# Kernel tuning notes

Measured on AMD Instinct MI355X. Metric: run time of the kernel, lower is better.

## Reference

```python
import jax, jax.numpy as jnp
import numpy as np

STD = 0.5
B = 1048576
DIM = 8  # arch == 2
_LOG_STD = -0.6931471805599453       # log(0.5)
_HALF_LOG_2PI = 0.9189385332046727   # 0.5*log(2*pi)


def _mlp(x, w1, b1, w2, b2):
    # Sequential(Linear, ReLU, Linear)
    return jnp.maximum(x @ w1 + b1, 0.0) @ w2 + b2


def _bce_sum(logits, targets):
    # BCEWithLogitsLoss(reduction='sum'), numerically stable
    return jnp.sum(jnp.maximum(logits, 0.0) - logits * targets
                   + jnp.log1p(jnp.exp(-jnp.abs(logits))))


def _normal_logprob_sum(mu, y):
    # D.Normal(mu, STD).log_prob(y).sum()
    return jnp.sum(-0.5 * ((y - mu) / STD) ** 2 - _LOG_STD - _HALF_LOG_2PI)


def setup_inputs() -> dict:
    key = jax.random.key(0)
    keys = iter(jax.random.split(key, 64))

    def nrm(shape, s=1.0):
        return s * jax.random.normal(next(keys), shape, dtype=jnp.float32)

    inp = {
        'y1': nrm((B, 1)),
        'y2': nrm((B, 1)),
        'n1': jax.random.uniform(next(keys), (B, 2), dtype=jnp.float32),
        'n2': jax.random.uniform(next(keys), (B, 2), dtype=jnp.float32),
        'n3': jax.random.uniform(next(keys), (B, 2), dtype=jnp.float32),
        'n4': jax.random.uniform(next(keys), (B, 2), dtype=jnp.float32),
    }
    # (name, d_in, d_out) for every 2-layer MLP in infnet/gennet
    mlp_specs = [('inf0', 2, 2), ('inf1', 3, 2), ('inf2', 1, 2), ('inf3', 2, 2),
                 ('g1', 2, 2), ('g2', 2, 1), ('g3', 1, 2), ('g4', 2, 2), ('g5', 2, 1)]
    for name, din, dout in mlp_specs:
        inp[name + '_w1'] = nrm((din, DIM), 0.5)
        inp[name + '_b1'] = nrm((DIM,), 0.1)
        inp[name + '_w2'] = nrm((DIM, dout), 0.5)
        inp[name + '_b2'] = nrm((dout,), 0.1)
    inp['g0_w'] = nrm((1, 2), 0.5)  # gennet[0]: Linear(1, z, bias=False)
    return inp


def reference(y1, y2, n1, n2, n3, n4,
              inf0_w1, inf0_b1, inf0_w2, inf0_b2,
              inf1_w1, inf1_b1, inf1_w2, inf1_b2,
              inf2_w1, inf2_b1, inf2_w2, inf2_b2,
              inf3_w1, inf3_b1, inf3_w2, inf3_b2,
              g1_w1, g1_b1, g1_w2, g1_b2,
              g2_w1, g2_b1, g2_w2, g2_b2,
              g3_w1, g3_b1, g3_w2, g3_b2,
              g4_w1, g4_b1, g4_w2, g4_b2,
              g5_w1, g5_b1, g5_w2, g5_b2,
              g0_w):
    b = y1.shape[0]
    # ---- infer(): recognition pass with hard Bernoulli samples ----
    pz1 = jax.nn.sigmoid(_mlp(jnp.concatenate([y1, y2], axis=1),
                              inf0_w1, inf0_b1, inf0_w2, inf0_b2))
    z1 = (pz1 > n1).astype(jnp.float32)
    pz2 = jax.nn.sigmoid(_mlp(jnp.concatenate([y2, z1], axis=1),
                              inf1_w1, inf1_b1, inf1_w2, inf1_b2))
    z2 = (pz2 > n2).astype(jnp.float32)
    pz3 = jax.nn.sigmoid(_mlp(y2, inf2_w1, inf2_b1, inf2_w2, inf2_b2))
    z3 = (pz3 > n3).astype(jnp.float32)
    pz4 = jax.nn.sigmoid(_mlp(z3, inf3_w1, inf3_b1, inf3_w2, inf3_b2))
    z4 = (pz4 > n4).astype(jnp.float32)
    # ---- generate_wake(): generative logits conditioned on inferred latents ----
    l4 = jnp.ones((b, 1), jnp.float32) @ g0_w          # [B, 2]
    l3 = _mlp(z4, g1_w1, g1_b1, g1_w2, g1_b2)          # [B, 2]
    muy2 = _mlp(z3, g2_w1, g2_b1, g2_w2, g2_b2)        # [B, 1]
    l2 = _mlp(y2, g3_w1, g3_b1, g3_w2, g3_b2)          # [B, 2]
    l1 = _mlp(z2, g4_w1, g4_b1, g4_w2, g4_b2)          # [B, 2]
    muy1 = _mlp(z1, g5_w1, g5_b1, g5_w2, g5_b2)        # [B, 1]
    # ---- wake losses ----
    bf = jnp.float32(b)
    loss_z = (_bce_sum(l1, z1) + _bce_sum(l2, z2)
              + _bce_sum(l3, z3) + _bce_sum(l4, z4)) / bf
    loss_y = (-_normal_logprob_sum(muy1, y1)
              - _normal_logprob_sum(muy2, y2)) / bf
    return (loss_z + loss_y, loss_z, loss_y)
```

## Files before the change

kernel.cpp:

```cpp
#include <hip/hip_runtime.h>

#define NB 1024
#define NT 256

__device__ __forceinline__ float bce_f(float l, float t) {
    float e = __expf(-fabsf(l));
    return fmaxf(l, 0.0f) - l * t + __logf(1.0f + e);
}

__device__ __forceinline__ float z_from(float s, float n) {
    float e = __expf(-s);
    return (1.0f - n > n * e) ? 1.0f : 0.0f;
}

__global__ __launch_bounds__(NT) void wake_main(
    const float* __restrict__ y1, const float* __restrict__ y2,
    const float* __restrict__ n1, const float* __restrict__ n2,
    const float* __restrict__ n3, const float* __restrict__ n4,
    const float* __restrict__ i0w1, const float* __restrict__ i0b1,
    const float* __restrict__ i0w2, const float* __restrict__ i0b2,
    const float* __restrict__ i1w1, const float* __restrict__ i1b1,
    const float* __restrict__ i1w2, const float* __restrict__ i1b2,
    const float* __restrict__ i2w1, const float* __restrict__ i2b1,
    const float* __restrict__ i2w2, const float* __restrict__ i2b2,
    const float* __restrict__ i3w1, const float* __restrict__ i3b1,
    const float* __restrict__ i3w2, const float* __restrict__ i3b2,
    const float* __restrict__ g1w1, const float* __restrict__ g1b1,
    const float* __restrict__ g1w2, const float* __restrict__ g1b2,
    const float* __restrict__ g2w1, const float* __restrict__ g2b1,
    const float* __restrict__ g2w2, const float* __restrict__ g2b2,
    const float* __restrict__ g3w1, const float* __restrict__ g3b1,
    const float* __restrict__ g3w2, const float* __restrict__ g3b2,
    const float* __restrict__ g4w1, const float* __restrict__ g4b1,
    const float* __restrict__ g4w2, const float* __restrict__ g4b2,
    const float* __restrict__ g5w1, const float* __restrict__ g5b1,
    const float* __restrict__ g5w2, const float* __restrict__ g5b2,
    const float* __restrict__ g0w,
    float2* __restrict__ partials)
{
    __shared__ float lds_eval[5][4][2];
    __shared__ float lds_coef[40];

    const int tid = threadIdx.x;
    const int g = blockIdx.x * NT + tid;

    const float4 vy1  = reinterpret_cast<const float4*>(y1)[g];
    const float4 vy2  = reinterpret_cast<const float4*>(y2)[g];
    const float4 n1lo = reinterpret_cast<const float4*>(n1)[2*g];
    const float4 n1hi = reinterpret_cast<const float4*>(n1)[2*g+1];
    const float4 n2lo = reinterpret_cast<const float4*>(n2)[2*g];
    const float4 n2hi = reinterpret_cast<const float4*>(n2)[2*g+1];
    const float4 n3lo = reinterpret_cast<const float4*>(n3)[2*g];
    const float4 n3hi = reinterpret_cast<const float4*>(n3)[2*g+1];
    const float4 n4lo = reinterpret_cast<const float4*>(n4)[2*g];
    const float4 n4hi = reinterpret_cast<const float4*>(n4)[2*g+1];

    if (tid < 20) {
        const int m = tid >> 2, c = tid & 3;
        const float z0 = (float)(c & 1), z1f = (float)(c >> 1);
        const float *w1, *bb1, *w2, *bb2; int dout;
        switch (m) {
            case 0:  w1 = i3w1; bb1 = i3b1; w2 = i3w2; bb2 = i3b2; dout = 2; break;
            case 1:  w1 = g1w1; bb1 = g1b1; w2 = g1w2; bb2 = g1b2; dout = 2; break;
            case 2:  w1 = g2w1; bb1 = g2b1; w2 = g2w2; bb2 = g2b2; dout = 1; break;
            case 3:  w1 = g4w1; bb1 = g4b1; w2 = g4w2; bb2 = g4b2; dout = 2; break;
            default: w1 = g5w1; bb1 = g5b1; w2 = g5w2; bb2 = g5b2; dout = 1; break;
        }
        float o0 = bb2[0];
        float o1 = (dout == 2) ? bb2[1] : 0.0f;
        #pragma unroll
        for (int j = 0; j < 8; ++j) {
            float h = fmaxf(bb1[j] + z0 * w1[j] + z1f * w1[8 + j], 0.0f);
            o0 += h * w2[j * dout];
            if (dout == 2) o1 += h * w2[j * 2 + 1];
        }
        lds_eval[m][c][0] = o0;
        lds_eval[m][c][1] = o1;
    }
    __syncthreads();
    if (tid < 10) {
        const int m = tid >> 1, k = tid & 1;
        const float f00 = lds_eval[m][0][k], f10 = lds_eval[m][1][k];
        const float f01 = lds_eval[m][2][k], f11 = lds_eval[m][3][k];
        lds_coef[tid * 4 + 0] = f00;
        lds_coef[tid * 4 + 1] = f10 - f00;
        lds_coef[tid * 4 + 2] = f01 - f00;
        lds_coef[tid * 4 + 3] = f11 - f10 - f01 + f00;
    }
    __syncthreads();

    const float l40 = g0w[0], l41 = g0w[1];

    const float Y1a[4] = {vy1.x, vy1.y, vy1.z, vy1.w};
    const float Y2a[4] = {vy2.x, vy2.y, vy2.z, vy2.w};
    const float N1a[8] = {n1lo.x, n1lo.y, n1lo.z, n1lo.w, n1hi.x, n1hi.y, n1hi.z, n1hi.w};
    const float N2a[8] = {n2lo.x, n2lo.y, n2lo.z, n2lo.w, n2hi.x, n2hi.y, n2hi.z, n2hi.w};
    const float N3a[8] = {n3lo.x, n3lo.y, n3lo.z, n3lo.w, n3hi.x, n3hi.y, n3hi.z, n3hi.w};
    const float N4a[8] = {n4lo.x, n4lo.y, n4lo.z, n4lo.w, n4hi.x, n4hi.y, n4hi.z, n4hi.w};

    float lz = 0.0f, ly = 0.0f;
    #pragma unroll
    for (int s = 0; s < 4; ++s) {
        const float Y1 = Y1a[s], Y2 = Y2a[s];
        float s10 = i0b2[0], s11 = i0b2[1];
        #pragma unroll
        for (int j = 0; j < 8; ++j) {
            float h = fmaxf(i0b1[j] + Y1 * i0w1[j] + Y2 * i0w1[8 + j], 0.0f);
            s10 += h * i0w2[2 * j]; s11 += h * i0w2[2 * j + 1];
        }
        const float z10 = z_from(s10, N1a[2 * s]);
        const float z11 = z_from(s11, N1a[2 * s + 1]);
        float s20 = i1b2[0], s21 = i1b2[1];
        #pragma unroll
        for (int j = 0; j < 8; ++j) {
            float h = fmaxf(i1b1[j] + Y2 * i1w1[j] + z10 * i1w1[8 + j] + z11 * i1w1[16 + j], 0.0f);
            s20 += h * i1w2[2 * j]; s21 += h * i1w2[2 * j + 1];
        }
        const float z20 = z_from(s20, N2a[2 * s]);
        const float z21 = z_from(s21, N2a[2 * s + 1]);
        float s30 = i2b2[0], s31 = i2b2[1];
        #pragma unroll
        for (int j = 0; j < 8; ++j) {
            float h = fmaxf(i2b1[j] + Y2 * i2w1[j], 0.0f);
            s30 += h * i2w2[2 * j]; s31 += h * i2w2[2 * j + 1];
        }
        const float z30 = z_from(s30, N3a[2 * s]);
        const float z31 = z_from(s31, N3a[2 * s + 1]);
        const float p3 = z30 * z31;
        const float s40 = lds_coef[0] + lds_coef[1] * z30 + lds_coef[2] * z31 + lds_coef[3] * p3;
        const float s41 = lds_coef[4] + lds_coef[5] * z30 + lds_coef[6] * z31 + lds_coef[7] * p3;
        const float z40 = z_from(s40, N4a[2 * s]);
        const float z41 = z_from(s41, N4a[2 * s + 1]);
        const float p4 = z40 * z41;
        const float l30 = lds_coef[8]  + lds_coef[9]  * z40 + lds_coef[10] * z41 + lds_coef[11] * p4;
        const float l31 = lds_coef[12] + lds_coef[13] * z40 + lds_coef[14] * z41 + lds_coef[15] * p4;
        const float muy2 = lds_coef[16] + lds_coef[17] * z30 + lds_coef[18] * z31 + lds_coef[19] * p3;
        float l20 = g3b2[0], l21 = g3b2[1];
        #pragma unroll
        for (int j = 0; j < 8; ++j) {
            float h = fmaxf(g3b1[j] + Y2 * g3w1[j], 0.0f);
            l20 += h * g3w2[2 * j]; l21 += h * g3w2[2 * j + 1];
        }
        const float p2 = z20 * z21;
        const float l10 = lds_coef[24] + lds_coef[25] * z20 + lds_coef[26] * z21 + lds_coef[27] * p2;
        const float l11 = lds_coef[28] + lds_coef[29] * z20 + lds_coef[30] * z21 + lds_coef[31] * p2;
        const float p1 = z10 * z11;
        const float muy1 = lds_coef[32] + lds_coef[33] * z10 + lds_coef[34] * z11 + lds_coef[35] * p1;

        lz += bce_f(l10, z10) + bce_f(l11, z11)
            + bce_f(l20, z20) + bce_f(l21, z21)
            + bce_f(l30, z30) + bce_f(l31, z31)
            - l40 * z40 - l41 * z41;
        const float d1 = Y1 - muy1, d2 = Y2 - muy2;
        ly += 2.0f * (d1 * d1) + 2.0f * (d2 * d2);
    }

    #pragma unroll
    for (int off = 32; off > 0; off >>= 1) {
        lz += __shfl_down(lz, off);
        ly += __shfl_down(ly, off);
    }
    __shared__ float2 wsum[NT / 64];
    const int lane = tid & 63, wid = tid >> 6;
    if (lane == 0) wsum[wid] = make_float2(lz, ly);
    __syncthreads();
    if (tid == 0) {
        float a = 0.0f, b = 0.0f;
        #pragma unroll
        for (int w = 0; w < NT / 64; ++w) { a += wsum[w].x; b += wsum[w].y; }
        partials[blockIdx.x] = make_float2(a, b);
    }
}

__global__ __launch_bounds__(256) void wake_reduce(
    const float2* __restrict__ partials, const float* __restrict__ g0w,
    float* __restrict__ out)
{
    const int tid = threadIdx.x;
    float lz = 0.0f, ly = 0.0f;
    #pragma unroll
    for (int i = 0; i < NB / 256; ++i) {
        float2 p = partials[tid + i * 256];
        lz += p.x; ly += p.y;
    }
    #pragma unroll
    for (int off = 32; off > 0; off >>= 1) {
        lz += __shfl_down(lz, off);
        ly += __shfl_down(ly, off);
    }
    __shared__ float2 wsum[4];
    const int lane = tid & 63, wid = tid >> 6;
    if (lane == 0) wsum[wid] = make_float2(lz, ly);
    __syncthreads();
    if (tid == 0) {
        float a = 0.0f, b = 0.0f;
        #pragma unroll
        for (int w = 0; w < 4; ++w) { a += wsum[w].x; b += wsum[w].y; }
        const float l40 = g0w[0], l41 = g0w[1];
        const float C4 = fmaxf(l40, 0.0f) + __logf(1.0f + __expf(-fabsf(l40)))
                       + fmaxf(l41, 0.0f) + __logf(1.0f + __expf(-fabsf(l41)));
        const float inv = 1.0f / 1048576.0f;
        const float loss_z = a * inv + C4;
        const float loss_y = b * inv + 0.4515827052894548f;
        out[0] = loss_z + loss_y;
        out[1] = loss_z;
        out[2] = loss_y;
    }
}

extern "C" void kernel_launch(void* const* d_in, const int* in_sizes, int n_in,
                              void* d_out, int out_size, void* d_ws, size_t ws_size,
                              hipStream_t stream) {
    const float* p[43];
    for (int i = 0; i < 43; ++i) p[i] = (const float*)d_in[i];
    float2* partials = (float2*)d_ws;
    wake_main<<<NB, NT, 0, stream>>>(
        p[0], p[1], p[2], p[3], p[4], p[5],
        p[6], p[7], p[8], p[9],
        p[10], p[11], p[12], p[13],
        p[14], p[15], p[16], p[17],
        p[18], p[19], p[20], p[21],
        p[22], p[23], p[24], p[25],
        p[26], p[27], p[28], p[29],
        p[30], p[31], p[32], p[33],
        p[34], p[35], p[36], p[37],
        p[38], p[39], p[40], p[41],
        p[42], partials);
    wake_reduce<<<1, 256, 0, stream>>>(partials, p[42], (float*)d_out);
}
```

Before: 26.56 us.

## Fuse final reduction into main kernel and precompute sigmoid/softplus lookup tables

The separate reduce kernel is removed; the last block to finish, found through an atomic counter, does the final reduction, and a memset resets the counter before each launch. The grid doubles to 2048 blocks with 2 samples per thread, and the per-sample math is rewritten with packed float2 vectors. The bilinear tables over binary latents now hold sigmoid and softplus values precomputed per block, which removes per-sample exp/log for z4 and two of the BCE terms. The trade-offs are an extra memset launch and atomic traffic on the counter.

```diff
diff --git a/kernel.cpp b/kernel.cpp
--- a/kernel.cpp
+++ b/kernel.cpp
@@ -1,19 +1,78 @@
 #include <hip/hip_runtime.h>
-
-#define NB 1024
+#include <math.h>
+
+#define NBLK 2048
 #define NT 256
-
-__device__ __forceinline__ float bce_f(float l, float t) {
-    float e = __expf(-fabsf(l));
-    return fmaxf(l, 0.0f) - l * t + __logf(1.0f + e);
-}
-
-__device__ __forceinline__ float z_from(float s, float n) {
-    float e = __expf(-s);
-    return (1.0f - n > n * e) ? 1.0f : 0.0f;
-}
-
-__global__ __launch_bounds__(NT) void wake_main(
+#define CNT_OFF (NBLK * 8)
+
+typedef float f32x2 __attribute__((ext_vector_type(2)));
+
+__device__ __forceinline__ f32x2 relu2(f32x2 v) {
+    f32x2 z = {0.0f, 0.0f};
+    return __builtin_elementwise_max(v, z);
+}
+
+__device__ __forceinline__ f32x2 zpair(f32x2 s, f32x2 n) {
+    float ex = __expf(-s.x), ey = __expf(-s.y);
+    f32x2 r;
+    r.x = (1.0f - n.x > n.x * ex) ? 1.0f : 0.0f;
+    r.y = (1.0f - n.y > n.y * ey) ? 1.0f : 0.0f;
+    return r;
+}
+
+__device__ __forceinline__ float sp_f(float l) {
+    return fmaxf(l, 0.0f) + __logf(1.0f + __expf(-fabsf(l)));
+}
+
+__device__ __forceinline__ f32x2 bil(const f32x2* c, float z0, float z1, float p) {
+    return c[0] + z0 * c[1] + z1 * c[2] + p * c[3];
+}
+
+__device__ __forceinline__ f32x2 mlp1(const float* w1, const float* b1,
+                                      const float* w2, const float* b2, float x0) {
+    const f32x2* w1v = (const f32x2*)w1;
+    const f32x2* b1v = (const f32x2*)b1;
+    const f32x2* w2v = (const f32x2*)w2;
+    f32x2 acc = *(const f32x2*)b2;
+    #pragma unroll
+    for (int jp = 0; jp < 4; ++jp) {
+        f32x2 h = relu2(b1v[jp] + x0 * w1v[jp]);
+        acc += h.x * w2v[2 * jp] + h.y * w2v[2 * jp + 1];
+    }
+    return acc;
+}
+
+__device__ __forceinline__ f32x2 mlp2(const float* w1, const float* b1,
+                                      const float* w2, const float* b2,
+                                      float x0, float x1) {
+    const f32x2* w1v = (const f32x2*)w1;
+    const f32x2* b1v = (const f32x2*)b1;
+    const f32x2* w2v = (const f32x2*)w2;
+    f32x2 acc = *(const f32x2*)b2;
+    #pragma unroll
+    for (int jp = 0; jp < 4; ++jp) {
+        f32x2 h = relu2(b1v[jp] + x0 * w1v[jp] + x1 * w1v[4 + jp]);
+        acc += h.x * w2v[2 * jp] + h.y * w2v[2 * jp + 1];
+    }
+    return acc;
+}
+
+__device__ __forceinline__ f32x2 mlp3(const float* w1, const float* b1,
+                                      const float* w2, const float* b2,
+                                      float x0, float x1, float x2) {
+    const f32x2* w1v = (const f32x2*)w1;
+    const f32x2* b1v = (const f32x2*)b1;
+    const f32x2* w2v = (const f32x2*)w2;
+    f32x2 acc = *(const f32x2*)b2;
+    #pragma unroll
+    for (int jp = 0; jp < 4; ++jp) {
+        f32x2 h = relu2(b1v[jp] + x0 * w1v[jp] + x1 * w1v[4 + jp] + x2 * w1v[8 + jp]);
+        acc += h.x * w2v[2 * jp] + h.y * w2v[2 * jp + 1];
+    }
+    return acc;
+}
+
+__global__ __launch_bounds__(NT) void wake_fused(
     const float* __restrict__ y1, const float* __restrict__ y2,
     const float* __restrict__ n1, const float* __restrict__ n2,
     const float* __restrict__ n3, const float* __restrict__ n4,
@@ -36,24 +95,21 @@
     const float* __restrict__ g5w1, const float* __restrict__ g5b1,
     const float* __restrict__ g5w2, const float* __restrict__ g5b2,
     const float* __restrict__ g0w,
-    float2* __restrict__ partials)
+    float2* __restrict__ partials, unsigned* __restrict__ cnt,
+    float* __restrict__ out)
 {
     __shared__ float lds_eval[5][4][2];
-    __shared__ float lds_coef[40];
+    __shared__ __align__(8) float lds_coef[6][4][2];
 
     const int tid = threadIdx.x;
     const int g = blockIdx.x * NT + tid;
 
-    const float4 vy1  = reinterpret_cast<const float4*>(y1)[g];
-    const float4 vy2  = reinterpret_cast<const float4*>(y2)[g];
-    const float4 n1lo = reinterpret_cast<const float4*>(n1)[2*g];
-    const float4 n1hi = reinterpret_cast<const float4*>(n1)[2*g+1];
-    const float4 n2lo = reinterpret_cast<const float4*>(n2)[2*g];
-    const float4 n2hi = reinterpret_cast<const float4*>(n2)[2*g+1];
-    const float4 n3lo = reinterpret_cast<const float4*>(n3)[2*g];
-    const float4 n3hi = reinterpret_cast<const float4*>(n3)[2*g+1];
-    const float4 n4lo = reinterpret_cast<const float4*>(n4)[2*g];
-    const float4 n4hi = reinterpret_cast<const float4*>(n4)[2*g+1];
+    const f32x2 y1p = ((const f32x2*)y1)[g];
+    const f32x2 y2p = ((const f32x2*)y2)[g];
+    const float4 n1v = ((const float4*)n1)[g];
+    const float4 n2v = ((const float4*)n2)[g];
+    const float4 n3v = ((const float4*)n3)[g];
+    const float4 n4v = ((const float4*)n4)[g];
 
     if (tid < 20) {
         const int m = tid >> 2, c = tid & 3;
@@ -78,133 +134,145 @@
         lds_eval[m][c][1] = o1;
     }
     __syncthreads();
-    if (tid < 10) {
-        const int m = tid >> 1, k = tid & 1;
-        const float f00 = lds_eval[m][0][k], f10 = lds_eval[m][1][k];
-        const float f01 = lds_eval[m][2][k], f11 = lds_eval[m][3][k];
-        lds_coef[tid * 4 + 0] = f00;
-        lds_coef[tid * 4 + 1] = f10 - f00;
-        lds_coef[tid * 4 + 2] = f01 - f00;
-        lds_coef[tid * 4 + 3] = f11 - f10 - f01 + f00;
-    }
-    __syncthreads();
-
-    const float l40 = g0w[0], l41 = g0w[1];
-
-    const float Y1a[4] = {vy1.x, vy1.y, vy1.z, vy1.w};
-    const float Y2a[4] = {vy2.x, vy2.y, vy2.z, vy2.w};
-    const float N1a[8] = {n1lo.x, n1lo.y, n1lo.z, n1lo.w, n1hi.x, n1hi.y, n1hi.z, n1hi.w};
-    const float N2a[8] = {n2lo.x, n2lo.y, n2lo.z, n2lo.w, n2hi.x, n2hi.y, n2hi.z, n2hi.w};
-    const float N3a[8] = {n3lo.x, n3lo.y, n3lo.z, n3lo.w, n3hi.x, n3hi.y, n3hi.z, n3hi.w};
-    const float N4a[8] = {n4lo.x, n4lo.y, n4lo.z, n4lo.w, n4hi.x, n4hi.y, n4hi.z, n4hi.w};
-
-    float lz = 0.0f, ly = 0.0f;
-    #pragma unroll
-    for (int s = 0; s < 4; ++s) {
+    if (tid < 12) {
+        const int pair = tid >> 1, elem = tid & 1;
+        int m, k, tf;
+        switch (tid) {
+            case 0:  m = 0; k = 0; tf = 1; break;
+            case 1:  m = 0; k = 1; tf = 1; break;
+            case 2:  m = 1; k = 0; tf = 0; break;
+            case 3:  m = 1; k = 1; tf = 0; break;
+            case 4:  m = 1; k = 0; tf = 2; break;
+            case 5:  m = 1; k = 1; tf = 2; break;
+            case 6:  m = 3; k = 0; tf = 0; break;
+            case 7:  m = 3; k = 1; tf = 0; break;
+            case 8:  m = 3; k = 0; tf = 2; break;
+            case 9:  m = 3; k = 1; tf = 2; break;
+            case 10: m = 2; k = 0; tf = 0; break;
+            default: m = 4; k = 0; tf = 0; break;
+        }
+        float f[4];
+        #pragma unroll
+        for (int c = 0; c < 4; ++c) {
+            float x = lds_eval[m][c][k];
+            if (tf == 1)      x = 1.0f / (1.0f + __expf(-x));
+            else if (tf == 2) x = fmaxf(x, 0.0f) + log1pf(__expf(-fabsf(x)));
+            f[c] = x;
+        }
+        lds_coef[pair][0][elem] = f[0];
+        lds_coef[pair][1][elem] = f[1] - f[0];
+        lds_coef[pair][2][elem] = f[2] - f[0];
+        lds_coef[pair][3][elem] = f[3] - f[1] - f[2] + f[0];
+    }
+    __syncthreads();
+
+    f32x2 C[6][4];
+    #pragma unroll
+    for (int pq = 0; pq < 24; ++pq)
+        C[pq >> 2][pq & 3] = *(const f32x2*)&lds_coef[pq >> 2][pq & 3][0];
+    const float L40 = g0w[0], L41 = g0w[1];
+
+    const float Y1a[2] = {y1p.x, y1p.y};
+    const float Y2a[2] = {y2p.x, y2p.y};
+    f32x2 N1a[2], N2a[2], N3a[2], N4a[2];
+    N1a[0].x = n1v.x; N1a[0].y = n1v.y; N1a[1].x = n1v.z; N1a[1].y = n1v.w;
+    N2a[0].x = n2v.x; N2a[0].y = n2v.y; N2a[1].x = n2v.z; N2a[1].y = n2v.w;
+    N3a[0].x = n3v.x; N3a[0].y = n3v.y; N3a[1].x = n3v.z; N3a[1].y = n3v.w;
+    N4a[0].x = n4v.x; N4a[0].y = n4v.y; N4a[1].x = n4v.z; N4a[1].y = n4v.w;
+
+    float lz = 0.0f;
+    f32x2 lyv = {0.0f, 0.0f};
+    #pragma unroll
+    for (int s = 0; s < 2; ++s) {
         const float Y1 = Y1a[s], Y2 = Y2a[s];
-        float s10 = i0b2[0], s11 = i0b2[1];
-        #pragma unroll
-        for (int j = 0; j < 8; ++j) {
-            float h = fmaxf(i0b1[j] + Y1 * i0w1[j] + Y2 * i0w1[8 + j], 0.0f);
-            s10 += h * i0w2[2 * j]; s11 += h * i0w2[2 * j + 1];
-        }
-        const float z10 = z_from(s10, N1a[2 * s]);
-        const float z11 = z_from(s11, N1a[2 * s + 1]);
-        float s20 = i1b2[0], s21 = i1b2[1];
-        #pragma unroll
-        for (int j = 0; j < 8; ++j) {
-            float h = fmaxf(i1b1[j] + Y2 * i1w1[j] + z10 * i1w1[8 + j] + z11 * i1w1[16 + j], 0.0f);
-            s20 += h * i1w2[2 * j]; s21 += h * i1w2[2 * j + 1];
-        }
-        const float z20 = z_from(s20, N2a[2 * s]);
-        const float z21 = z_from(s21, N2a[2 * s + 1]);
-        float s30 = i2b2[0], s31 = i2b2[1];
-        #pragma unroll
-        for (int j = 0; j < 8; ++j) {
-            float h = fmaxf(i2b1[j] + Y2 * i2w1[j], 0.0f);
-            s30 += h * i2w2[2 * j]; s31 += h * i2w2[2 * j + 1];
-        }
-        const float z30 = z_from(s30, N3a[2 * s]);
-        const float z31 = z_from(s31, N3a[2 * s + 1]);
-        const float p3 = z30 * z31;
-        const float s40 = lds_coef[0] + lds_coef[1] * z30 + lds_coef[2] * z31 + lds_coef[3] * p3;
-        const float s41 = lds_coef[4] + lds_coef[5] * z30 + lds_coef[6] * z31 + lds_coef[7] * p3;
-        const float z40 = z_from(s40, N4a[2 * s]);
-        const float z41 = z_from(s41, N4a[2 * s + 1]);
-        const float p4 = z40 * z41;
-        const float l30 = lds_coef[8]  + lds_coef[9]  * z40 + lds_coef[10] * z41 + lds_coef[11] * p4;
-        const float l31 = lds_coef[12] + lds_coef[13] * z40 + lds_coef[14] * z41 + lds_coef[15] * p4;
-        const float muy2 = lds_coef[16] + lds_coef[17] * z30 + lds_coef[18] * z31 + lds_coef[19] * p3;
-        float l20 = g3b2[0], l21 = g3b2[1];
-        #pragma unroll
-        for (int j = 0; j < 8; ++j) {
-            float h = fmaxf(g3b1[j] + Y2 * g3w1[j], 0.0f);
-            l20 += h * g3w2[2 * j]; l21 += h * g3w2[2 * j + 1];
-        }
-        const float p2 = z20 * z21;
-        const float l10 = lds_coef[24] + lds_coef[25] * z20 + lds_coef[26] * z21 + lds_coef[27] * p2;
-        const float l11 = lds_coef[28] + lds_coef[29] * z20 + lds_coef[30] * z21 + lds_coef[31] * p2;
-        const float p1 = z10 * z11;
-        const float muy1 = lds_coef[32] + lds_coef[33] * z10 + lds_coef[34] * z11 + lds_coef[35] * p1;
-
-        lz += bce_f(l10, z10) + bce_f(l11, z11)
-            + bce_f(l20, z20) + bce_f(l21, z21)
-            + bce_f(l30, z30) + bce_f(l31, z31)
-            - l40 * z40 - l41 * z41;
-        const float d1 = Y1 - muy1, d2 = Y2 - muy2;
-        ly += 2.0f * (d1 * d1) + 2.0f * (d2 * d2);
-    }
-
+        f32x2 s1 = mlp2(i0w1, i0b1, i0w2, i0b2, Y1, Y2);
+        f32x2 z1 = zpair(s1, N1a[s]);
+        f32x2 s2 = mlp3(i1w1, i1b1, i1w2, i1b2, Y2, z1.x, z1.y);
+        f32x2 z2 = zpair(s2, N2a[s]);
+        f32x2 s3 = mlp1(i2w1, i2b1, i2w2, i2b2, Y2);
+        f32x2 z3 = zpair(s3, N3a[s]);
+        const float p3 = z3.x * z3.y;
+        f32x2 sig4 = bil(C[0], z3.x, z3.y, p3);
+        f32x2 z4;
+        z4.x = (sig4.x > N4a[s].x) ? 1.0f : 0.0f;
+        z4.y = (sig4.y > N4a[s].y) ? 1.0f : 0.0f;
+        const float p4 = z4.x * z4.y;
+        f32x2 l3  = bil(C[1], z4.x, z4.y, p4);
+        f32x2 SP3 = bil(C[2], z4.x, z4.y, p4);
+        const float p2 = z2.x * z2.y;
+        f32x2 l1  = bil(C[3], z2.x, z2.y, p2);
+        f32x2 SP1 = bil(C[4], z2.x, z2.y, p2);
+        const float p1 = z1.x * z1.y;
+        f32x2 zA, zB, zP;
+        zA.x = z3.x; zA.y = z1.x;
+        zB.x = z3.y; zB.y = z1.y;
+        zP.x = p3;   zP.y = p1;
+        f32x2 mu = C[5][0] + zA * C[5][1] + zB * C[5][2] + zP * C[5][3];
+        f32x2 l2 = mlp1(g3w1, g3b1, g3w2, g3b2, Y2);
+        f32x2 bsum = (SP1 - l1 * z1) + (SP3 - l3 * z3);
+        f32x2 sp2;
+        sp2.x = sp_f(l2.x); sp2.y = sp_f(l2.y);
+        bsum += sp2 - l2 * z2;
+        lz += bsum.x + bsum.y - (L40 * z4.x + L41 * z4.y);
+        f32x2 d;
+        d.x = Y2 - mu.x; d.y = Y1 - mu.y;
+        lyv += d * d;
+    }
+
+    float lyf = lyv.x + lyv.y;
     #pragma unroll
     for (int off = 32; off > 0; off >>= 1) {
-        lz += __shfl_down(lz, off);
-        ly += __shfl_down(ly, off);
+        lz  += __shfl_down(lz, off);
+        lyf += __shfl_down(lyf, off);
     }
     __shared__ float2 wsum[NT / 64];
+    __shared__ int sflag;
     const int lane = tid & 63, wid = tid >> 6;
-    if (lane == 0) wsum[wid] = make_float2(lz, ly);
+    if (lane == 0) wsum[wid] = make_float2(lz, lyf);
     __syncthreads();
     if (tid == 0) {
         float a = 0.0f, b = 0.0f;
         #pragma unroll
         for (int w = 0; w < NT / 64; ++w) { a += wsum[w].x; b += wsum[w].y; }
-        partials[blockIdx.x] = make_float2(a, b);
-    }
-}
-
-__global__ __launch_bounds__(256) void wake_reduce(
-    const float2* __restrict__ partials, const float* __restrict__ g0w,
-    float* __restrict__ out)
-{
-    const int tid = threadIdx.x;
-    float lz = 0.0f, ly = 0.0f;
-    #pragma unroll
-    for (int i = 0; i < NB / 256; ++i) {
-        float2 p = partials[tid + i * 256];
-        lz += p.x; ly += p.y;
-    }
-    #pragma unroll
-    for (int off = 32; off > 0; off >>= 1) {
-        lz += __shfl_down(lz, off);
-        ly += __shfl_down(ly, off);
-    }
-    __shared__ float2 wsum[4];
-    const int lane = tid & 63, wid = tid >> 6;
-    if (lane == 0) wsum[wid] = make_float2(lz, ly);
-    __syncthreads();
-    if (tid == 0) {
+        union { float2 f; unsigned long long u; } pk;
+        pk.f = make_float2(a, b);
+        __hip_atomic_store((unsigned long long*)&partials[blockIdx.x], pk.u,
+                           __ATOMIC_RELEASE, __HIP_MEMORY_SCOPE_AGENT);
+        unsigned v = __hip_atomic_fetch_add(cnt, 1u, __ATOMIC_ACQ_REL,
+                                            __HIP_MEMORY_SCOPE_AGENT);
+        sflag = (v == NBLK - 1);
+    }
+    __syncthreads();
+    if (sflag) {
         float a = 0.0f, b = 0.0f;
         #pragma unroll
-        for (int w = 0; w < 4; ++w) { a += wsum[w].x; b += wsum[w].y; }
-        const float l40 = g0w[0], l41 = g0w[1];
-        const float C4 = fmaxf(l40, 0.0f) + __logf(1.0f + __expf(-fabsf(l40)))
-                       + fmaxf(l41, 0.0f) + __logf(1.0f + __expf(-fabsf(l41)));
-        const float inv = 1.0f / 1048576.0f;
-        const float loss_z = a * inv + C4;
-        const float loss_y = b * inv + 0.4515827052894548f;
-        out[0] = loss_z + loss_y;
-        out[1] = loss_z;
-        out[2] = loss_y;
+        for (int i = 0; i < NBLK / NT; ++i) {
+            union { float2 f; unsigned long long u; } q;
+            q.u = __hip_atomic_load((const unsigned long long*)&partials[tid + i * NT],
+                                    __ATOMIC_ACQUIRE, __HIP_MEMORY_SCOPE_AGENT);
+            a += q.f.x; b += q.f.y;
+        }
+        #pragma unroll
+        for (int off = 32; off > 0; off >>= 1) {
+            a += __shfl_down(a, off);
+            b += __shfl_down(b, off);
+        }
+        if (lane == 0) wsum[wid] = make_float2(a, b);
+        __syncthreads();
+        if (tid == 0) {
+            float sa = 0.0f, sb = 0.0f;
+            #pragma unroll
+            for (int w = 0; w < NT / 64; ++w) { sa += wsum[w].x; sb += wsum[w].y; }
+            const float l40 = g0w[0], l41 = g0w[1];
+            const float c4 = fmaxf(l40, 0.0f) + log1pf(expf(-fabsf(l40)))
+                           + fmaxf(l41, 0.0f) + log1pf(expf(-fabsf(l41)));
+            const float inv = 1.0f / 1048576.0f;
+            const float loss_z = sa * inv + c4;
+            const float loss_y = 2.0f * sb * inv + 0.4515827052894548f;
+            out[0] = loss_z + loss_y;
+            out[1] = loss_z;
+            out[2] = loss_y;
+        }
     }
 }
 
@@ -214,7 +282,9 @@
     const float* p[43];
     for (int i = 0; i < 43; ++i) p[i] = (const float*)d_in[i];
     float2* partials = (float2*)d_ws;
-    wake_main<<<NB, NT, 0, stream>>>(
+    unsigned* cnt = (unsigned*)((char*)d_ws + CNT_OFF);
+    hipMemsetAsync(cnt, 0, sizeof(unsigned), stream);
+    wake_fused<<<NBLK, NT, 0, stream>>>(
         p[0], p[1], p[2], p[3], p[4], p[5],
         p[6], p[7], p[8], p[9],
         p[10], p[11], p[12], p[13],
@@ -225,6 +295,5 @@
         p[30], p[31], p[32], p[33],
         p[34], p[35], p[36], p[37],
         p[38], p[39], p[40], p[41],
-        p[42], partials);
-    wake_reduce<<<1, 256, 0, stream>>>(partials, p[42], (float*)d_out);
-}
+        p[42], partials, cnt, (float*)d_out);
+}
```

New measurement: 84.36 us. 3.18x slower.
